# Kernel tuning notes

Hardware: AMD Instinct MI355X
Metric: run time of the kernel (lower is better)

The kernel has to match this reference:

```python
import jax, jax.numpy as jnp
import numpy as np

LAYERS = 3
N_NODES = 100000
N_EDGES = 800000
EMB = 100
EPS = 1e-12  # F.normalize default eps


def setup_inputs() -> dict:
    key = jax.random.key(0)
    ks = jax.random.split(key, 7)
    embedding = jax.random.normal(ks[0], (N_NODES, EMB), dtype=jnp.float32)
    adj_val = jax.random.uniform(ks[1], (N_EDGES,), dtype=jnp.float32)
    w_att = jax.random.normal(ks[2], (EMB, 1), dtype=jnp.float32) * 0.1
    b_att = jax.random.normal(ks[3], (1,), dtype=jnp.float32) * 0.1
    w_items = jax.random.normal(ks[4], (LAYERS, EMB, EMB), dtype=jnp.float32) * 0.1
    adj_row = jax.random.randint(ks[5], (N_EDGES,), 0, N_NODES, dtype=jnp.int32)
    adj_col = jax.random.randint(ks[6], (N_EDGES,), 0, N_NODES, dtype=jnp.int32)
    return {"embedding": embedding, "adj_val": adj_val, "w_att": w_att,
            "b_att": b_att, "w_items": w_items, "adj_row": adj_row, "adj_col": adj_col}


def reference(embedding, adj_val, w_att, b_att, w_items, adj_row, adj_col):
    n = embedding.shape[0]
    # column-degree normalization: adjacency.multiply(1/adjacency.sum(axis=0))
    degree = jax.ops.segment_sum(adj_val, adj_col, num_segments=n)  # [N]
    vals = adj_val / degree[adj_col]  # per-edge normalized value

    x = embedding
    final = embedding
    for i in range(LAYERS):
        scores = x @ w_att + b_att              # [N,1]
        attw = jax.nn.softmax(scores, axis=0)   # softmax over nodes (dim=0)
        x = x @ w_items[i].T                    # nn.Linear (no bias)
        m = x * attw                            # attention-weighted features
        # sparse mm: out[r] = sum_{edges e: row[e]=r} vals[e] * m[col[e]]
        gathered = m[adj_col] * vals[:, None]   # [E, EMB]
        x = jax.ops.segment_sum(gathered, adj_row, num_segments=n)
        # F.normalize(p=2, dim=-1)
        norm = jnp.linalg.norm(x, axis=-1, keepdims=True)
        x = x / jnp.maximum(norm, EPS)
        final = final + x
    return final / (LAYERS + 1)
```

## Files before the change

### kernel.cpp

```cpp
#include <hip/hip_runtime.h>
#include <hip/hip_bf16.h>

#define NN 100000
#define NE 800000
#define EM 100
#define NL 3

typedef short bf16x8 __attribute__((ext_vector_type(8)));
typedef float f32x4  __attribute__((ext_vector_type(4)));
typedef unsigned long long u64;

#define GNE_C  3125
#define GW4_C  25000
#define GGE_C  1563
#define GCV_C  168

static constexpr size_t OFF_XB   = 0;
static constexpr size_t OFF_M    = OFF_XB   + (size_t)NN*128*2;
static constexpr size_t OFF_F    = OFF_M    + (size_t)NN*128;
static constexpr size_t OFF_DEG  = OFF_F    + (size_t)NN*EM*2;
static constexpr size_t OFF_SC   = OFF_DEG  + (size_t)NN*4;
static constexpr size_t OFF_ES   = OFF_SC   + (size_t)NN*4;
static constexpr size_t OFF_POS  = OFF_ES   + (size_t)NE*8;
static constexpr size_t OFF_CNT  = OFF_POS  + (size_t)NE*4;
static constexpr size_t OFF_DGF  = OFF_CNT  + (size_t)NN*4;
static constexpr size_t OFF_RP   = OFF_DGF  + (size_t)NN*8;
static constexpr size_t OFF_BS   = OFF_RP   + (size_t)(NN+64)*4;
static constexpr size_t OFF_FLAG = OFF_BS   + 512;
static constexpr size_t OFF_WAT  = OFF_FLAG + 16;
static constexpr size_t OFF_WBF  = OFF_WAT  + 512;
static constexpr size_t ZERO_BYTES = (size_t)NN*4 + (size_t)NN*8;

#define DEG_SCALE  4294967296.0f
#define DEG_INV    (1.0f/4294967296.0f)

__device__ inline float ldf(const void* p, int i, int f32) {
    return f32 ? ((const float*)p)[i]
               : __bfloat162float(((const __hip_bfloat16*)p)[i]);
}

__device__ inline float bflo(unsigned int u) { return __uint_as_float(u << 16); }
__device__ inline float bfhi(unsigned int u) { return __uint_as_float(u & 0xFFFF0000u); }
__device__ inline unsigned int pack2bf(float a, float b) {
    __hip_bfloat16 ha = __float2bfloat16(a), hb = __float2bfloat16(b);
    unsigned short ua = *(unsigned short*)&ha, ub = *(unsigned short*)&hb;
    return (unsigned int)ua | ((unsigned int)ub << 16);
}
__device__ inline float ub0(unsigned int x) { return (float)(x & 0xFF); }
__device__ inline float ub1(unsigned int x) { return (float)((x >> 8) & 0xFF); }
__device__ inline float ub2(unsigned int x) { return (float)((x >> 16) & 0xFF); }
__device__ inline float ub3(unsigned int x) { return (float)(x >> 24); }

__device__ inline int probe_block(const void* p, int nsamp) {
    __shared__ int sflag;
    int tid = threadIdx.x;
    if (tid < 64) {
        const unsigned short* h = (const unsigned short*)p;
        int big = 0;
        for (int i = tid; i < nsamp; i += 64) {
            int ex = (h[2 * i] >> 7) & 0xFF;
            big += (ex >= 134) ? 1 : 0;
        }
        #pragma unroll
        for (int off = 32; off; off >>= 1) big += __shfl_xor(big, off);
        if (tid == 0) sflag = (big >= 2) ? 1 : 0;
    }
    __syncthreads();
    int f = sflag;
    __syncthreads();
    return f;
}

__global__ __launch_bounds__(256) void k_init(const void* __restrict__ emb,
                                              const void* __restrict__ w_att,
                                              const void* __restrict__ w_itm,
                                              unsigned int* __restrict__ xbf,
                                              unsigned int* __restrict__ fin,
                                              float* __restrict__ scores, int* flags,
                                              float* __restrict__ wat,
                                              unsigned short* __restrict__ wbf) {
    int b = blockIdx.x;
    if (b < GW4_C) {
        int femb = probe_block(emb, 256);
        int fw = probe_block(w_att, 50);
        if (b == 0 && threadIdx.x == 0) flags[0] = femb;
        int lane = threadIdx.x & 63, w = threadIdx.x >> 6;
        int r = b * 4 + w;
        float f0 = 0.f, f1 = 0.f, part = 0.f;
        bool act = lane < 50;
        if (act) {
            if (femb) {
                float2 t = ((const float2*)emb)[(size_t)r * 50 + lane];
                f0 = t.x; f1 = t.y;
            } else {
                unsigned int u = ((const unsigned int*)emb)[(size_t)r * 50 + lane];
                f0 = bflo(u); f1 = bfhi(u);
            }
            float w0 = ldf(w_att, 2 * lane, fw);
            float w1 = ldf(w_att, 2 * lane + 1, fw);
            part = f0 * w0 + f1 * w1;
            fin[(size_t)r * 50 + lane] = pack2bf(f0, f1);
        }
        xbf[(size_t)r * 64 + lane] = act ? pack2bf(f0, f1) : 0u;
        #pragma unroll
        for (int off = 32; off; off >>= 1) part += __shfl_xor(part, off);
        if (lane == 0) scores[r] = expf(part);
    } else {
        int fw = probe_block(w_att, 50);
        int fi = probe_block(w_itm, 256);
        int i = (b - GW4_C) * 256 + threadIdx.x;
        if (i < 128) wat[i] = (i < EM) ? ldf(w_att, i, fw) : 0.f;
        if (i < NL * 112 * 128) {
            int l = i / (112 * 128), rem = i % (112 * 128);
            int n = rem >> 7, k = rem & 127;
            float v = (n < EM && k < EM) ? ldf(w_itm, (l * EM + n) * EM + k, fi) : 0.f;
            __hip_bfloat16 bb = __float2bfloat16(v);
            wbf[i] = *(unsigned short*)&bb;
        }
    }
}

__global__ __launch_bounds__(256) void k_deg(const void* __restrict__ val,
                                             const int* __restrict__ row, const int* __restrict__ col,
                                             u64* degfix, int* counts, int* __restrict__ pos) {
    int fav = probe_block(val, 256);
    int e = blockIdx.x * 256 + threadIdx.x;
    if (e >= NE) return;
    float v = ldf(val, e, fav);
    atomicAdd(&degfix[col[e]], (u64)llrintf(v * DEG_SCALE));
    pos[e] = atomicAdd(&counts[row[e]], 1);
}

__global__ __launch_bounds__(256) void k_scanA(const int* __restrict__ counts, int* excl, int* bsum,
                                               const u64* __restrict__ degfix, float* __restrict__ deg) {
    __shared__ int s[256];
    int base = blockIdx.x * 1024;
    int tid = threadIdx.x;
    int v[4]; int t = 0;
    #pragma unroll
    for (int i = 0; i < 4; i++) {
        int idx = base + tid * 4 + i;
        v[i] = (idx < NN) ? counts[idx] : 0;
        if (idx < NN) deg[idx] = (float)degfix[idx] * DEG_INV;
        t += v[i];
    }
    s[tid] = t; __syncthreads();
    for (int off = 1; off < 256; off <<= 1) {
        int add = (tid >= off) ? s[tid - off] : 0;
        __syncthreads();
        s[tid] += add;
        __syncthreads();
    }
    int ex = (tid == 0) ? 0 : s[tid - 1];
    #pragma unroll
    for (int i = 0; i < 4; i++) {
        int idx = base + tid * 4 + i;
        if (idx < NN) excl[idx] = ex;
        ex += v[i];
    }
    if (tid == 255) bsum[blockIdx.x] = s[255];
}

__global__ __launch_bounds__(256) void k_scanC(int* rowptr, const int* __restrict__ bsum) {
    __shared__ int spfx;
    int tid = threadIdx.x;
    int gi = blockIdx.x >> 2;
    if (tid < 64) {
        int t = (tid < gi) ? bsum[tid] : 0;
        if (tid + 64 < gi) t += bsum[tid + 64];
        #pragma unroll
        for (int off = 32; off; off >>= 1) t += __shfl_xor(t, off);
        if (tid == 0) spfx = t;
    }
    __syncthreads();
    int pfx = spfx;
    int i = blockIdx.x * 256 + tid;
    if (i < NN) {
        rowptr[i] += pfx;
        if (i == 0) rowptr[NN] = NE;
    }
}

__device__ void gemm_body(int gb, const unsigned short* __restrict__ xbf,
                          const unsigned short* __restrict__ wbf,
                          const float* __restrict__ scores,
                          const float* __restrict__ deg,
                          unsigned char* __restrict__ m, int layer) {
    int wid = threadIdx.x >> 6, lane = threadIdx.x & 63;
    int row0 = gb * 64 + wid * 16;
    if (row0 >= NN) return;
    int c15 = lane & 15, quad = lane >> 4;

    const bf16x8* xa = (const bf16x8*)(xbf + (size_t)(row0 + c15) * 128 + quad * 8);
    bf16x8 a[4];
    #pragma unroll
    for (int kq = 0; kq < 4; kq++) a[kq] = xa[kq * 4];

    float att[4];
    #pragma unroll
    for (int r = 0; r < 4; r++) {
        int grow = row0 + quad * 4 + r;
        float dv = deg[grow];
        float invd = dv > 0.f ? 1.0f / dv : 0.f;
        att[r] = scores[grow] * invd;
    }

    const bf16x8* wb = (const bf16x8*)(wbf + (size_t)layer * 112 * 128
                                       + (size_t)c15 * 128 + quad * 8);
    f32x4 accs[7];
    #pragma unroll
    for (int nt = 0; nt < 7; nt++) {
        f32x4 acc = {0.f, 0.f, 0.f, 0.f};
        #pragma unroll
        for (int kq = 0; kq < 4; kq++) {
            bf16x8 b = wb[nt * 256 + kq * 4];
            acc = __builtin_amdgcn_mfma_f32_16x16x32_bf16(a[kq], b, acc, 0, 0, 0);
        }
        accs[nt] = acc;
    }
    #pragma unroll
    for (int r = 0; r < 4; r++) {
        float mx = 0.f;
        #pragma unroll
        for (int nt = 0; nt < 7; nt++) mx = fmaxf(mx, fabsf(accs[nt][r]));
        #pragma unroll
        for (int off = 1; off < 16; off <<= 1) mx = fmaxf(mx, __shfl_xor(mx, off));
        float inv = 127.0f / fmaxf(mx, 1e-30f);
        int grow = row0 + quad * 4 + r;
        unsigned char* rowp = m + (size_t)grow * 128;
        #pragma unroll
        for (int nt = 0; nt < 7; nt++) {
            int col = nt * 16 + c15;
            if (col < EM) {
                int q = (int)rintf(accs[nt][r] * inv) + 128;
                rowp[col] = (unsigned char)q;
            }
        }
        if (c15 == 0) *(float*)(rowp + 100) = att[r] * mx * (1.0f / 127.0f);
        if (c15 < 6)  *(unsigned int*)(rowp + 104 + 4 * c15) = 0x80808080u;
    }
}

__global__ __launch_bounds__(256) void k_gemm(const unsigned short* __restrict__ xbf,
                                              const unsigned short* __restrict__ wbf,
                                              const float* __restrict__ scores,
                                              const float* __restrict__ deg,
                                              unsigned char* __restrict__ m, int layer) {
    gemm_body(blockIdx.x, xbf, wbf, scores, deg, m, layer);
}

__global__ __launch_bounds__(256) void k_sg(const int* __restrict__ row, const int* __restrict__ col,
                                            const void* __restrict__ aval,
                                            const int* __restrict__ rowptr,
                                            const int* __restrict__ pos, int2* __restrict__ es,
                                            const unsigned short* __restrict__ xbf,
                                            const unsigned short* __restrict__ wbf,
                                            const float* __restrict__ scores,
                                            const float* __restrict__ deg,
                                            unsigned char* __restrict__ m) {
    int b = blockIdx.x;
    if (b < GNE_C) {
        int fav = probe_block(aval, 256);
        int e = b * 256 + threadIdx.x;
        if (e >= NE) return;
        int p = rowptr[row[e]] + pos[e];
        es[p] = make_int2(col[e], __float_as_int(ldf(aval, e, fav)));
    } else {
        gemm_body(b - GNE_C, xbf, wbf, scores, deg, m, 0);
    }
}

__global__ __launch_bounds__(256) void k_spmm(const int* __restrict__ rowptr,
                                              const int2* __restrict__ es,
                                              const unsigned char* __restrict__ m,
                                              const float* __restrict__ wat,
                                              unsigned int* __restrict__ xbf,
                                              unsigned int* __restrict__ fin,
                                              float* __restrict__ scores,
                                              void* __restrict__ out, const int* flags,
                                              int last) {
    int lane = threadIdx.x & 63;
    int w = threadIdx.x >> 6;
    int r = blockIdx.x * 4 + w;
    int slot = lane >> 4, k = lane & 15;
    int s = rowptr[r], e = rowptr[r + 1];
    const char* mq = (const char*)m;
    int src12 = (lane & 48) + 12;

    float acc[8] = {0.f, 0.f, 0.f, 0.f, 0.f, 0.f, 0.f, 0.f};
    float tsum = 0.f;
    for (int i = s; i < e; i += 8) {
        int i0 = i + slot, i1 = i + 4 + slot;
        int j0 = i0 < e - 1 ? i0 : e - 1;
        int j1 = i1 < e - 1 ? i1 : e - 1;
        int2 c0 = es[j0];
        int2 c1 = es[j1];
        float v0 = (i0 < e) ? __int_as_float(c0.y) : 0.f;
        float v1 = (i1 < e) ? __int_as_float(c1.y) : 0.f;
        uint2 u0 = *(const uint2*)(mq + (((size_t)c0.x) << 7) + (k << 3));
        uint2 u1 = *(const uint2*)(mq + (((size_t)c1.x) << 7) + (k << 3));
        float s0 = __uint_as_float(__shfl((int)u0.y, src12));
        float s1 = __uint_as_float(__shfl((int)u1.y, src12));
        float t0 = v0 * s0, t1 = v1 * s1;
        tsum += t0 + t1;
        unsigned int x0 = u0.x, y0 = (k == 12) ? 0x80808080u : u0.y;
        unsigned int x1 = u1.x, y1 = (k == 12) ? 0x80808080u : u1.y;
        acc[0] += t0 * ub0(x0); acc[1] += t0 * ub1(x0);
        acc[2] += t0 * ub2(x0); acc[3] += t0 * ub3(x0);
        acc[4] += t0 * ub0(y0); acc[5] += t0 * ub1(y0);
        acc[6] += t0 * ub2(y0); acc[7] += t0 * ub3(y0);
        acc[0] += t1 * ub0(x1); acc[1] += t1 * ub1(x1);
        acc[2] += t1 * ub2(x1); acc[3] += t1 * ub3(x1);
        acc[4] += t1 * ub0(y1); acc[5] += t1 * ub1(y1);
        acc[6] += t1 * ub2(y1); acc[7] += t1 * ub3(y1);
    }
    #pragma unroll
    for (int t = 0; t < 8; t++) {
        acc[t] += __shfl_xor(acc[t], 16);
        acc[t] += __shfl_xor(acc[t], 32);
    }
    tsum += __shfl_xor(tsum, 16);
    tsum += __shfl_xor(tsum, 32);
    float corr = 128.0f * tsum;
    #pragma unroll
    for (int t = 0; t < 8; t++) acc[t] -= corr;

    float sq = 0.f;
    #pragma unroll
    for (int t = 0; t < 8; t++) sq += acc[t] * acc[t];
    #pragma unroll
    for (int off = 8; off; off >>= 1) sq += __shfl_xor(sq, off);
    float rn = 1.f / fmaxf(sqrtf(sq), 1e-12f);
    float n[8];
    #pragma unroll
    for (int t = 0; t < 8; t++) n[t] = acc[t] * rn;

    float part = 0.f;
    if (slot == 0) {
        if (!last) {
            uint4 q;
            q.x = pack2bf(n[0], n[1]); q.y = pack2bf(n[2], n[3]);
            q.z = pack2bf(n[4], n[5]); q.w = pack2bf(n[6], n[7]);
            *(uint4*)(xbf + (size_t)r * 64 + k * 4) = q;
        }
        if (k <= 12) {
            unsigned int fu[4] = {0u, 0u, 0u, 0u};
            size_t fb = (size_t)r * 50 + k * 4;
            uint2 fa = *(const uint2*)(fin + fb);
            fu[0] = fa.x; fu[1] = fa.y;
            if (k < 12) {
                uint2 fbv = *(const uint2*)(fin + fb + 2);
                fu[2] = fbv.x; fu[3] = fbv.y;
            }
            float fn[8];
            #pragma unroll
            for (int t = 0; t < 4; t++) {
                fn[2 * t]     = bflo(fu[t]) + n[2 * t];
                fn[2 * t + 1] = bfhi(fu[t]) + n[2 * t + 1];
            }
            if (!last) {
                uint2 pa, pb;
                pa.x = pack2bf(fn[0], fn[1]); pa.y = pack2bf(fn[2], fn[3]);
                pb.x = pack2bf(fn[4], fn[5]); pb.y = pack2bf(fn[6], fn[7]);
                *(uint2*)(fin + fb) = pa;
                if (k < 12) *(uint2*)(fin + fb + 2) = pb;
                float4 w0 = *(const float4*)(wat + k * 8);
                float4 w1 = *(const float4*)(wat + k * 8 + 4);
                part = n[0] * w0.x + n[1] * w0.y + n[2] * w0.z + n[3] * w0.w
                     + n[4] * w1.x + n[5] * w1.y + n[6] * w1.z + n[7] * w1.w;
            } else {
                if (flags[0]) {
                    float4 A, B;
                    A.x = fn[0] * 0.25f; A.y = fn[1] * 0.25f; A.z = fn[2] * 0.25f; A.w = fn[3] * 0.25f;
                    B.x = fn[4] * 0.25f; B.y = fn[5] * 0.25f; B.z = fn[6] * 0.25f; B.w = fn[7] * 0.25f;
                    float* ob = (float*)out + (size_t)r * 100 + k * 8;
                    *(float4*)ob = A;
                    if (k < 12) *(float4*)(ob + 4) = B;
                } else {
                    uint2 pa, pb;
                    pa.x = pack2bf(fn[0] * 0.25f, fn[1] * 0.25f);
                    pa.y = pack2bf(fn[2] * 0.25f, fn[3] * 0.25f);
                    pb.x = pack2bf(fn[4] * 0.25f, fn[5] * 0.25f);
                    pb.y = pack2bf(fn[6] * 0.25f, fn[7] * 0.25f);
                    unsigned int* ob = (unsigned int*)out + (size_t)r * 50 + k * 4;
                    *(uint2*)ob = pa;
                    if (k < 12) *(uint2*)(ob + 2) = pb;
                }
            }
        }
    }
    if (!last) {
        #pragma unroll
        for (int off = 8; off; off >>= 1) part += __shfl_xor(part, off);
        if (lane == 0) scores[r] = expf(part);
    }
}

extern "C" void kernel_launch(void* const* d_in, const int* in_sizes, int n_in,
                              void* d_out, int out_size, void* d_ws, size_t ws_size,
                              hipStream_t stream) {
    const void* emb   = d_in[0];
    const void* aval  = d_in[1];
    const void* w_att = d_in[2];
    const void* w_itm = d_in[4];
    const int* arow = (const int*)d_in[5];
    const int* acol = (const int*)d_in[6];

    char* w = (char*)d_ws;
    unsigned int*   xbf    = (unsigned int*)(w + OFF_XB);
    unsigned char*  m      = (unsigned char*)(w + OFF_M);
    unsigned int*   fin    = (unsigned int*)(w + OFF_F);
    float*          deg    = (float*)(w + OFF_DEG);
    float*          scores = (float*)(w + OFF_SC);
    int2*           es     = (int2*) (w + OFF_ES);
    int*            pos    = (int*)  (w + OFF_POS);
    int*            counts = (int*)  (w + OFF_CNT);
    u64*            degfix = (u64*)  (w + OFF_DGF);
    int*            rowptr = (int*)  (w + OFF_RP);
    int*            bsum   = (int*)  (w + OFF_BS);
    int*            flags  = (int*)  (w + OFF_FLAG);
    float*          wat    = (float*)(w + OFF_WAT);
    unsigned short* wbf    = (unsigned short*)(w + OFF_WBF);

    const int GN   = (NN + 255) / 256;
    const int GSCN = (NN + 1023) / 1024;
    const int GINI = GW4_C + GCV_C;
    const int GSG  = GNE_C + GGE_C;

    hipMemsetAsync(w + OFF_CNT, 0, ZERO_BYTES, stream);

    k_init<<<GINI, 256, 0, stream>>>(emb, w_att, w_itm, xbf, fin, scores, flags,
                                     wat, wbf);
    k_deg<<<GNE_C, 256, 0, stream>>>(aval, arow, acol, degfix, counts, pos);
    k_scanA<<<GSCN, 256, 0, stream>>>(counts, rowptr, bsum, degfix, deg);
    k_scanC<<<GN, 256, 0, stream>>>(rowptr, bsum);
    k_sg<<<GSG, 256, 0, stream>>>(arow, acol, aval, rowptr, pos, es,
                                  (const unsigned short*)xbf, wbf, scores, deg, m);

    k_spmm<<<GW4_C, 256, 0, stream>>>(rowptr, es, m, wat, xbf, fin, scores,
                                      d_out, flags, 0);
    for (int l = 1; l < NL; l++) {
        k_gemm<<<GGE_C, 256, 0, stream>>>((const unsigned short*)xbf, wbf, scores, deg, m, l);
        k_spmm<<<GW4_C, 256, 0, stream>>>(rowptr, es, m, wat, xbf, fin, scores,
                                          d_out, flags, (l == NL - 1) ? 1 : 0);
    }
}
```

Baseline: 475.0 us.

## Widen SpMM gathers to 16-byte loads and fold memset into init kernel

The SpMM kernel now has each lane load 16 bytes of a gathered uint8 feature row, so 8 lanes cover a row and each wave handles 8 edges per slot instead of 4. This halves the number of gather instructions per row and changes the reduction and shuffle pattern. Separately, the hipMemsetAsync that zeroed the counts and degree buffers is replaced by extra blocks in k_init that write zeros, removing one launch. The cost is higher register pressure from 16 accumulators, and the epilogue's writes are now concentrated in fewer lanes.

Result: slower. 546.2 us (+15.0%).

```diff
diff --git a/kernel.cpp b/kernel.cpp
--- a/kernel.cpp
+++ b/kernel.cpp
@@ -14,6 +14,7 @@
 #define GW4_C  25000
 #define GGE_C  1563
 #define GCV_C  168
+#define GZR_C  293
 
 static constexpr size_t OFF_XB   = 0;
 static constexpr size_t OFF_M    = OFF_XB   + (size_t)NN*128*2;
@@ -29,7 +30,6 @@
 static constexpr size_t OFF_FLAG = OFF_BS   + 512;
 static constexpr size_t OFF_WAT  = OFF_FLAG + 16;
 static constexpr size_t OFF_WBF  = OFF_WAT  + 512;
-static constexpr size_t ZERO_BYTES = (size_t)NN*4 + (size_t)NN*8;
 
 #define DEG_SCALE  4294967296.0f
 #define DEG_INV    (1.0f/4294967296.0f)
@@ -78,7 +78,8 @@
                                               unsigned int* __restrict__ fin,
                                               float* __restrict__ scores, int* flags,
                                               float* __restrict__ wat,
-                                              unsigned short* __restrict__ wbf) {
+                                              unsigned short* __restrict__ wbf,
+                                              unsigned int* __restrict__ zbase) {
     int b = blockIdx.x;
     if (b < GW4_C) {
         int femb = probe_block(emb, 256);
@@ -105,7 +106,7 @@
         #pragma unroll
         for (int off = 32; off; off >>= 1) part += __shfl_xor(part, off);
         if (lane == 0) scores[r] = expf(part);
-    } else {
+    } else if (b < GW4_C + GCV_C) {
         int fw = probe_block(w_att, 50);
         int fi = probe_block(w_itm, 256);
         int i = (b - GW4_C) * 256 + threadIdx.x;
@@ -117,6 +118,9 @@
             __hip_bfloat16 bb = __float2bfloat16(v);
             wbf[i] = *(unsigned short*)&bb;
         }
+    } else {
+        int i = (b - GW4_C - GCV_C) * 256 + threadIdx.x;
+        if (i < 75000) ((uint4*)zbase)[i] = make_uint4(0u, 0u, 0u, 0u);
     }
 }
 
@@ -282,116 +286,138 @@
     int lane = threadIdx.x & 63;
     int w = threadIdx.x >> 6;
     int r = blockIdx.x * 4 + w;
-    int slot = lane >> 4, k = lane & 15;
+    int slot = lane >> 3, k8 = lane & 7;
     int s = rowptr[r], e = rowptr[r + 1];
     const char* mq = (const char*)m;
-    int src12 = (lane & 48) + 12;
-
-    float acc[8] = {0.f, 0.f, 0.f, 0.f, 0.f, 0.f, 0.f, 0.f};
+    int src6 = (lane & 56) + 6;
+
+    float acc[16];
+    #pragma unroll
+    for (int t = 0; t < 16; t++) acc[t] = 0.f;
     float tsum = 0.f;
-    for (int i = s; i < e; i += 8) {
-        int i0 = i + slot, i1 = i + 4 + slot;
+    for (int i = s; i < e; i += 16) {
+        int i0 = i + slot, i1 = i + 8 + slot;
         int j0 = i0 < e - 1 ? i0 : e - 1;
         int j1 = i1 < e - 1 ? i1 : e - 1;
         int2 c0 = es[j0];
         int2 c1 = es[j1];
         float v0 = (i0 < e) ? __int_as_float(c0.y) : 0.f;
         float v1 = (i1 < e) ? __int_as_float(c1.y) : 0.f;
-        uint2 u0 = *(const uint2*)(mq + (((size_t)c0.x) << 7) + (k << 3));
-        uint2 u1 = *(const uint2*)(mq + (((size_t)c1.x) << 7) + (k << 3));
-        float s0 = __uint_as_float(__shfl((int)u0.y, src12));
-        float s1 = __uint_as_float(__shfl((int)u1.y, src12));
+        uint4 u0 = *(const uint4*)(mq + (((size_t)c0.x) << 7) + (k8 << 4));
+        uint4 u1 = *(const uint4*)(mq + (((size_t)c1.x) << 7) + (k8 << 4));
+        float s0 = __uint_as_float(__shfl((int)u0.y, src6));
+        float s1 = __uint_as_float(__shfl((int)u1.y, src6));
         float t0 = v0 * s0, t1 = v1 * s1;
         tsum += t0 + t1;
-        unsigned int x0 = u0.x, y0 = (k == 12) ? 0x80808080u : u0.y;
-        unsigned int x1 = u1.x, y1 = (k == 12) ? 0x80808080u : u1.y;
-        acc[0] += t0 * ub0(x0); acc[1] += t0 * ub1(x0);
-        acc[2] += t0 * ub2(x0); acc[3] += t0 * ub3(x0);
-        acc[4] += t0 * ub0(y0); acc[5] += t0 * ub1(y0);
-        acc[6] += t0 * ub2(y0); acc[7] += t0 * ub3(y0);
-        acc[0] += t1 * ub0(x1); acc[1] += t1 * ub1(x1);
-        acc[2] += t1 * ub2(x1); acc[3] += t1 * ub3(x1);
-        acc[4] += t1 * ub0(y1); acc[5] += t1 * ub1(y1);
-        acc[6] += t1 * ub2(y1); acc[7] += t1 * ub3(y1);
-    }
-    #pragma unroll
-    for (int t = 0; t < 8; t++) {
+        if (k8 == 6) { u0.y = 0x80808080u; u1.y = 0x80808080u; }
+        const unsigned int* p0 = (const unsigned int*)&u0;
+        const unsigned int* p1 = (const unsigned int*)&u1;
+        #pragma unroll
+        for (int q = 0; q < 4; q++) {
+            acc[4*q+0] += t0 * ub0(p0[q]); acc[4*q+1] += t0 * ub1(p0[q]);
+            acc[4*q+2] += t0 * ub2(p0[q]); acc[4*q+3] += t0 * ub3(p0[q]);
+        }
+        #pragma unroll
+        for (int q = 0; q < 4; q++) {
+            acc[4*q+0] += t1 * ub0(p1[q]); acc[4*q+1] += t1 * ub1(p1[q]);
+            acc[4*q+2] += t1 * ub2(p1[q]); acc[4*q+3] += t1 * ub3(p1[q]);
+        }
+    }
+    #pragma unroll
+    for (int t = 0; t < 16; t++) {
+        acc[t] += __shfl_xor(acc[t], 8);
         acc[t] += __shfl_xor(acc[t], 16);
         acc[t] += __shfl_xor(acc[t], 32);
     }
+    tsum += __shfl_xor(tsum, 8);
     tsum += __shfl_xor(tsum, 16);
     tsum += __shfl_xor(tsum, 32);
     float corr = 128.0f * tsum;
     #pragma unroll
-    for (int t = 0; t < 8; t++) acc[t] -= corr;
+    for (int t = 0; t < 16; t++) acc[t] -= corr;
 
     float sq = 0.f;
     #pragma unroll
-    for (int t = 0; t < 8; t++) sq += acc[t] * acc[t];
-    #pragma unroll
-    for (int off = 8; off; off >>= 1) sq += __shfl_xor(sq, off);
+    for (int t = 0; t < 16; t++) sq += acc[t] * acc[t];
+    sq += __shfl_xor(sq, 4);
+    sq += __shfl_xor(sq, 2);
+    sq += __shfl_xor(sq, 1);
     float rn = 1.f / fmaxf(sqrtf(sq), 1e-12f);
-    float n[8];
-    #pragma unroll
-    for (int t = 0; t < 8; t++) n[t] = acc[t] * rn;
+    float n[16];
+    #pragma unroll
+    for (int t = 0; t < 16; t++) n[t] = acc[t] * rn;
 
     float part = 0.f;
     if (slot == 0) {
         if (!last) {
-            uint4 q;
-            q.x = pack2bf(n[0], n[1]); q.y = pack2bf(n[2], n[3]);
-            q.z = pack2bf(n[4], n[5]); q.w = pack2bf(n[6], n[7]);
-            *(uint4*)(xbf + (size_t)r * 64 + k * 4) = q;
-        }
-        if (k <= 12) {
-            unsigned int fu[4] = {0u, 0u, 0u, 0u};
-            size_t fb = (size_t)r * 50 + k * 4;
-            uint2 fa = *(const uint2*)(fin + fb);
-            fu[0] = fa.x; fu[1] = fa.y;
-            if (k < 12) {
-                uint2 fbv = *(const uint2*)(fin + fb + 2);
-                fu[2] = fbv.x; fu[3] = fbv.y;
-            }
-            float fn[8];
+            uint4 qa, qb;
+            qa.x = pack2bf(n[0], n[1]);   qa.y = pack2bf(n[2], n[3]);
+            qa.z = pack2bf(n[4], n[5]);   qa.w = pack2bf(n[6], n[7]);
+            qb.x = pack2bf(n[8], n[9]);   qb.y = pack2bf(n[10], n[11]);
+            qb.z = pack2bf(n[12], n[13]); qb.w = pack2bf(n[14], n[15]);
+            uint4* xb = (uint4*)(xbf + (size_t)r * 64 + lane * 8);
+            xb[0] = qa; xb[1] = qb;
             #pragma unroll
-            for (int t = 0; t < 4; t++) {
-                fn[2 * t]     = bflo(fu[t]) + n[2 * t];
-                fn[2 * t + 1] = bfhi(fu[t]) + n[2 * t + 1];
+            for (int t = 0; t < 16; t += 4) {
+                float4 wv = *(const float4*)(wat + lane * 16 + t);
+                part += n[t] * wv.x + n[t+1] * wv.y + n[t+2] * wv.z + n[t+3] * wv.w;
+            }
+        }
+        if (lane < 7) {
+            size_t fb = (size_t)r * 50 + lane * 8;
+            int nu = (lane < 6) ? 8 : 2;
+            unsigned int fu[8] = {0u,0u,0u,0u,0u,0u,0u,0u};
+            #pragma unroll
+            for (int t = 0; t < 8; t += 2) {
+                if (t < nu) { uint2 p = *(const uint2*)(fin + fb + t); fu[t] = p.x; fu[t+1] = p.y; }
+            }
+            float fn[16];
+            #pragma unroll
+            for (int t = 0; t < 8; t++) {
+                fn[2*t]   = bflo(fu[t]) + n[2*t];
+                fn[2*t+1] = bfhi(fu[t]) + n[2*t+1];
             }
             if (!last) {
-                uint2 pa, pb;
-                pa.x = pack2bf(fn[0], fn[1]); pa.y = pack2bf(fn[2], fn[3]);
-                pb.x = pack2bf(fn[4], fn[5]); pb.y = pack2bf(fn[6], fn[7]);
-                *(uint2*)(fin + fb) = pa;
-                if (k < 12) *(uint2*)(fin + fb + 2) = pb;
-                float4 w0 = *(const float4*)(wat + k * 8);
-                float4 w1 = *(const float4*)(wat + k * 8 + 4);
-                part = n[0] * w0.x + n[1] * w0.y + n[2] * w0.z + n[3] * w0.w
-                     + n[4] * w1.x + n[5] * w1.y + n[6] * w1.z + n[7] * w1.w;
+                #pragma unroll
+                for (int t = 0; t < 8; t += 2) {
+                    if (t < nu) {
+                        uint2 p;
+                        p.x = pack2bf(fn[2*t],   fn[2*t+1]);
+                        p.y = pack2bf(fn[2*t+2], fn[2*t+3]);
+                        *(uint2*)(fin + fb + t) = p;
+                    }
+                }
             } else {
                 if (flags[0]) {
-                    float4 A, B;
-                    A.x = fn[0] * 0.25f; A.y = fn[1] * 0.25f; A.z = fn[2] * 0.25f; A.w = fn[3] * 0.25f;
-                    B.x = fn[4] * 0.25f; B.y = fn[5] * 0.25f; B.z = fn[6] * 0.25f; B.w = fn[7] * 0.25f;
-                    float* ob = (float*)out + (size_t)r * 100 + k * 8;
-                    *(float4*)ob = A;
-                    if (k < 12) *(float4*)(ob + 4) = B;
+                    float* ob = (float*)out + (size_t)r * 100 + lane * 16;
+                    #pragma unroll
+                    for (int t = 0; t < 16; t += 4) {
+                        if (t < 2 * nu) {
+                            float4 A;
+                            A.x = fn[t]   * 0.25f; A.y = fn[t+1] * 0.25f;
+                            A.z = fn[t+2] * 0.25f; A.w = fn[t+3] * 0.25f;
+                            *(float4*)(ob + t) = A;
+                        }
+                    }
                 } else {
-                    uint2 pa, pb;
-                    pa.x = pack2bf(fn[0] * 0.25f, fn[1] * 0.25f);
-                    pa.y = pack2bf(fn[2] * 0.25f, fn[3] * 0.25f);
-                    pb.x = pack2bf(fn[4] * 0.25f, fn[5] * 0.25f);
-                    pb.y = pack2bf(fn[6] * 0.25f, fn[7] * 0.25f);
-                    unsigned int* ob = (unsigned int*)out + (size_t)r * 50 + k * 4;
-                    *(uint2*)ob = pa;
-                    if (k < 12) *(uint2*)(ob + 2) = pb;
+                    unsigned int* ob = (unsigned int*)out + (size_t)r * 50 + lane * 8;
+                    #pragma unroll
+                    for (int t = 0; t < 8; t += 2) {
+                        if (t < nu) {
+                            uint2 p;
+                            p.x = pack2bf(fn[2*t]   * 0.25f, fn[2*t+1] * 0.25f);
+                            p.y = pack2bf(fn[2*t+2] * 0.25f, fn[2*t+3] * 0.25f);
+                            *(uint2*)(ob + t) = p;
+                        }
+                    }
                 }
             }
         }
     }
     if (!last) {
-        #pragma unroll
-        for (int off = 8; off; off >>= 1) part += __shfl_xor(part, off);
+        part += __shfl_xor(part, 4);
+        part += __shfl_xor(part, 2);
+        part += __shfl_xor(part, 1);
         if (lane == 0) scores[r] = expf(part);
     }
 }
@@ -424,13 +450,11 @@
 
     const int GN   = (NN + 255) / 256;
     const int GSCN = (NN + 1023) / 1024;
-    const int GINI = GW4_C + GCV_C;
+    const int GINI = GW4_C + GCV_C + GZR_C;
     const int GSG  = GNE_C + GGE_C;
 
-    hipMemsetAsync(w + OFF_CNT, 0, ZERO_BYTES, stream);
-
     k_init<<<GINI, 256, 0, stream>>>(emb, w_att, w_itm, xbf, fin, scores, flags,
-                                     wat, wbf);
+                                     wat, wbf, (unsigned int*)(w + OFF_CNT));
     k_deg<<<GNE_C, 256, 0, stream>>>(aval, arow, acol, degfix, counts, pos);
     k_scanA<<<GSCN, 256, 0, stream>>>(counts, rowptr, bsum, degfix, deg);
     k_scanC<<<GN, 256, 0, stream>>>(rowptr, bsum);
```
